# Performance work log

Measured on AMD Instinct MI355X. Metric: run time of the kernel, lower is better.

The kernel has to match this reference:

```python
import jax, jax.numpy as jnp
import numpy as np

B, S, D, H = 8, 1024, 512, 8
HD = D // H
EPS = 1e-5


def layer_norm(x, g, b):
    m = jnp.mean(x, axis=-1, keepdims=True)
    v = jnp.mean(jnp.square(x - m), axis=-1, keepdims=True)
    return (x - m) * jax.lax.rsqrt(v + EPS) * g + b


def mha(x, w_in, b_in, w_out, b_out):
    # x: [B,S,D]; w_in: [3D,D]; PyTorch MultiheadAttention math (no dropout, eval)
    b, s, d = x.shape
    qkv = x @ w_in.T + b_in                      # [B,S,3D]
    q, k, v = jnp.split(qkv, 3, axis=-1)
    q = q.reshape(b, s, H, HD)
    k = k.reshape(b, s, H, HD)
    v = v.reshape(b, s, H, HD)
    scores = jnp.einsum('bqhd,bkhd->bhqk', q, k) / np.sqrt(HD)
    a = jax.nn.softmax(scores, axis=-1)
    o = jnp.einsum('bhqk,bkhd->bqhd', a, v).reshape(b, s, d)
    return o @ w_out.T + b_out


def interp_linear(y, out_size):
    # y: [B,S_in,D]; torch F.interpolate(mode='linear', align_corners=False)
    s_in = y.shape[1]
    scale = s_in / out_size
    src = (jnp.arange(out_size, dtype=jnp.float32) + 0.5) * scale - 0.5
    src = jnp.clip(src, 0.0, s_in - 1.0)
    i0 = jnp.floor(src).astype(jnp.int32)
    i1 = jnp.minimum(i0 + 1, s_in - 1)
    w = (src - i0.astype(jnp.float32))[None, :, None]
    return y[:, i0, :] * (1.0 - w) + y[:, i1, :] * w


def setup_inputs() -> dict:
    key = jax.random.key(0)
    ks = jax.random.split(key, 16)
    sd = 0.02
    return {
        'x': jax.random.normal(ks[0], (B, S, D), jnp.float32),
        'w_in1': jax.random.normal(ks[1], (3 * D, D), jnp.float32) * sd,
        'b_in1': jnp.zeros((3 * D,), jnp.float32),
        'w_out1': jax.random.normal(ks[2], (D, D), jnp.float32) * sd,
        'b_out1': jnp.zeros((D,), jnp.float32),
        'w_in2': jax.random.normal(ks[3], (3 * D, D), jnp.float32) * sd,
        'b_in2': jnp.zeros((3 * D,), jnp.float32),
        'w_out2': jax.random.normal(ks[4], (D, D), jnp.float32) * sd,
        'b_out2': jnp.zeros((D,), jnp.float32),
        'g1': jnp.ones((D,), jnp.float32), 'beta1': jnp.zeros((D,), jnp.float32),
        'g2': jnp.ones((D,), jnp.float32), 'beta2': jnp.zeros((D,), jnp.float32),
        'g3': jnp.ones((D,), jnp.float32), 'beta3': jnp.zeros((D,), jnp.float32),
        'w_ff1': jax.random.normal(ks[5], (4 * D, D), jnp.float32) * sd,
        'b_ff1': jnp.zeros((4 * D,), jnp.float32),
        'w_ff2': jax.random.normal(ks[6], (D, 4 * D), jnp.float32) * sd,
        'b_ff2': jnp.zeros((D,), jnp.float32),
    }


def reference(x, w_in1, b_in1, w_out1, b_out1, w_in2, b_in2, w_out2, b_out2,
              g1, beta1, g2, beta2, g3, beta3, w_ff1, b_ff1, w_ff2, b_ff2):
    a1 = mha(x, w_in1, b_in1, w_out1, b_out1)
    x = layer_norm(x + a1, g1, beta1)
    # avg_pool1d kernel=2 stride=2 ceil_mode (S even -> exact halving)
    pooled = x.reshape(B, S // 2, 2, D).mean(axis=2)
    a2 = mha(pooled, w_in2, b_in2, w_out2, b_out2)
    up = interp_linear(a2, S)
    x = layer_norm(x + up, g2, beta2)
    h = jax.nn.gelu(x @ w_ff1.T + b_ff1, approximate=False)
    ff = h @ w_ff2.T + b_ff2
    return layer_norm(x + ff, g3, beta3)
```

## Files before the change

### kernel.cpp

```cpp
#include <hip/hip_runtime.h>
#include <hip/hip_bf16.h>
#include <math.h>

typedef __hip_bfloat16 bf16;
typedef __attribute__((ext_vector_type(8))) short short8;
typedef __attribute__((ext_vector_type(4))) float f32x4;
typedef __attribute__((ext_vector_type(16))) float f32x16;

__device__ __forceinline__ float ldf(const float* p, size_t i) { return p[i]; }
__device__ __forceinline__ float ldf(const bf16*  p, size_t i) { return __bfloat162float(p[i]); }
__device__ __forceinline__ void  stf(float* p, size_t i, float v) { p[i] = v; }
__device__ __forceinline__ void  stf(bf16*  p, size_t i, float v) { p[i] = __float2bfloat16(v); }

__device__ __forceinline__ float ex2(float x) { return __builtin_amdgcn_exp2f(x); }

__device__ __forceinline__ void gl16(const void* gp, void* lp) {
    __builtin_amdgcn_global_load_lds(
        (const __attribute__((address_space(1))) void*)gp,
        (__attribute__((address_space(3))) void*)lp, 16, 0, 0);
}

__device__ __forceinline__ void pl32swap(unsigned &a, unsigned &b) {
    asm volatile("v_permlane32_swap_b32 %0, %1" : "+v"(a), "+v"(b));
}

__global__ __launch_bounds__(256) void cvt_all(
    const float* __restrict__ x,
    const float* __restrict__ s0, const float* __restrict__ s1,
    const float* __restrict__ s2, const float* __restrict__ s3,
    const float* __restrict__ s4, const float* __restrict__ s5,
    bf16* __restrict__ dst)
{
    int i = blockIdx.x * 256 + threadIdx.x;
    if (i < 4194304) {
        dst[i] = __float2bfloat16(x[i]);
        return;
    }
    int j = i - 4194304;
    const float* s; int off;
    if      (j <  786432) { s = s0; off = 0; }
    else if (j < 1048576) { s = s1; off =  786432; }
    else if (j < 1835008) { s = s2; off = 1048576; }
    else if (j < 2097152) { s = s3; off = 1835008; }
    else if (j < 3145728) { s = s4; off = 2097152; }
    else                  { s = s5; off = 3145728; }
    dst[i] = __float2bfloat16(s[j - off]);
}

template <int EPI, int BN, int VS>
__global__ __launch_bounds__(256) void gemm_rs(
    const bf16* __restrict__ A, const bf16* __restrict__ W,
    const float* __restrict__ bias, bf16* __restrict__ C,
    bf16* __restrict__ vt, int M, int N, int K)
{
    constexpr int WNC = BN / 2;
    constexpr int NT  = BN / 32;
    constexpr int RB  = BN / 32;

    __shared__ __align__(16) bf16 Asl[2][128 * 64];
    __shared__ __align__(16) bf16 Bsl[2][BN * 64];

    const int tid  = threadIdx.x;
    const int lane = tid & 63;
    const int wave = tid >> 6;
    const int wm   = wave >> 1, wn = wave & 1;
    const int l15  = lane & 15, quad = lane >> 4;

    const int nwg = gridDim.x * gridDim.y;
    const int bid = blockIdx.y * gridDim.x + blockIdx.x;
    const int wid = (bid & 7) * (nwg >> 3) + (bid >> 3);
    const int bx  = wid % gridDim.x, by = wid / gridDim.x;
    const int row0 = by * 128, col0 = bx * BN;

    const int sr = tid >> 3;
    const int gg = tid & 7;

    const bf16* As[4]; const bf16* Ws[RB]; int loA[4], loB[RB];
    #pragma unroll
    for (int j = 0; j < 4; j++) {
        int row = j * 32 + sr;
        int gs  = (gg ^ (row & 7)) * 8;
        As[j]  = &A[(size_t)(row0 + row) * K + gs];
        loA[j] = row * 64 + gg * 8;
    }
    #pragma unroll
    for (int j = 0; j < RB; j++) {
        int row = j * 32 + sr;
        int gs  = (gg ^ (row & 7)) * 8;
        Ws[j]  = &W[(size_t)(col0 + row) * K + gs];
        loB[j] = row * 64 + gg * 8;
    }

    short8 ga[4], gb[RB];
    auto LOADG = [&](int k0) {
        #pragma unroll
        for (int j = 0; j < 4; j++) ga[j] = *(const short8*)(As[j] + k0);
        #pragma unroll
        for (int j = 0; j < RB; j++) gb[j] = *(const short8*)(Ws[j] + k0);
    };
    auto WRITEL = [&](int buf) {
        #pragma unroll
        for (int j = 0; j < 4; j++) *(short8*)&Asl[buf][loA[j]] = ga[j];
        #pragma unroll
        for (int j = 0; j < RB; j++) *(short8*)&Bsl[buf][loB[j]] = gb[j];
    };

    f32x4 acc[4][NT] = {};
    const int nk = K >> 6;

    LOADG(0);
    WRITEL(0);
    __syncthreads();

    int cur = 0;
    for (int i = 0; i < nk; i++) {
        if (i + 1 < nk) LOADG((i + 1) << 6);

        #pragma unroll
        for (int ks = 0; ks < 64; ks += 32) {
            short8 af[4], bfr[NT];
            const int g0 = (ks >> 3) + quad;
            const int col = (g0 ^ (l15 & 7)) * 8;
            #pragma unroll
            for (int mt = 0; mt < 4; mt++)
                af[mt] = *(const short8*)&Asl[cur][(wm * 64 + mt * 16 + l15) * 64 + col];
            #pragma unroll
            for (int nt = 0; nt < NT; nt++)
                bfr[nt] = *(const short8*)&Bsl[cur][(wn * WNC + nt * 16 + l15) * 64 + col];
            #pragma unroll
            for (int mt = 0; mt < 4; mt++)
                #pragma unroll
                for (int nt = 0; nt < NT; nt++)
                    acc[mt][nt] = __builtin_amdgcn_mfma_f32_16x16x32_bf16(
                        af[mt], bfr[nt], acc[mt][nt], 0, 0, 0);
        }

        if (i + 1 < nk) WRITEL(cur ^ 1);
        __syncthreads();
        cur ^= 1;
    }

    if constexpr (VS > 0) {
        if (col0 >= 1024) {
            constexpr int LS = (VS == 1024) ? 10 : 9;
            #pragma unroll
            for (int mt = 0; mt < 4; mt++) {
                int rowm = row0 + wm * 64 + mt * 16 + quad * 4;
                int b8 = rowm >> LS;
                int s4 = rowm & (VS - 1);
                #pragma unroll
                for (int nt = 0; nt < NT; nt++) {
                    int col = col0 + wn * WNC + nt * 16 + l15;
                    float bv = bias[col];
                    int hd = col - 1024;
                    union { bf16 b4[4]; unsigned long long u; } pk;
                    #pragma unroll
                    for (int r = 0; r < 4; r++)
                        pk.b4[r] = __float2bfloat16(acc[mt][nt][r] + bv);
                    *(unsigned long long*)&vt[
                        ((size_t)(b8 * 8 + (hd >> 6)) * 64 + (hd & 63)) * VS + s4] = pk.u;
                }
            }
            return;
        }
    }

    #pragma unroll
    for (int mt = 0; mt < 4; mt++) {
        int row = row0 + wm * 64 + mt * 16 + quad * 4;
        #pragma unroll
        for (int nt = 0; nt < NT; nt++) {
            int col = col0 + wn * WNC + nt * 16 + l15;
            float bv = bias[col];
            #pragma unroll
            for (int r = 0; r < 4; r++) {
                float v = acc[mt][nt][r] + bv;
                if (EPI == 1) v = 0.5f * v * (1.0f + erff(v * 0.70710678118654752f));
                C[(size_t)(row + r) * N + col] = __float2bfloat16(v);
            }
        }
    }
}

template <int LQB>
__global__ __launch_bounds__(128) void flash_attn_mfma(
    const bf16* __restrict__ qkv, const bf16* __restrict__ vt,
    bf16* __restrict__ o)
{
    constexpr int S   = 64 << LQB;
    constexpr int nt2 = 1 << (LQB - 1);

    __shared__ __align__(16) bf16 Kl[2][128 * 64];

    const int tid  = threadIdx.x;
    const int wave = tid >> 6, lane = tid & 63;
    const int l31  = lane & 31, hi = lane >> 5;

    const int r    = blockIdx.x;
    const int w    = (r & 7) * ((1 << LQB) * 8) + (r >> 3);
    const int qblk = w & ((1 << LQB) - 1);
    const int bh   = w >> LQB;
    const int h    = bh & 7, bb = bh >> 3;
    const int q0   = qblk * 64 + wave * 32;

    const bf16* base  = qkv + (size_t)bb * S * 1536 + h * 64;
    const bf16* vbase = vt + (size_t)bh * 64 * S;

    short8 qf[4];
    #pragma unroll
    for (int c = 0; c < 4; c++)
        qf[c] = *(const short8*)&base[(size_t)(q0 + l31) * 1536 + c * 16 + hi * 8];

    const int sr = lane >> 3;
    const int sc = ((lane & 7) ^ sr) * 8;

    auto STGK = [&](int buf, int j) {
        #pragma unroll
        for (int t = 0; t < 8; t++) {
            int r0 = wave * 64 + t * 8;
            gl16(&base[(size_t)((j << 7) + r0 + sr) * 1536 + 512 + sc],
                 &Kl[buf][r0 * 64]);
        }
    };

    f32x16 oacc[2] = {};
    float lrow = 0.f;
    const float CE = 0.18033688f;

    STGK(0, 0);

    for (int j = 0; j < nt2; j++) {
        const int cur = j & 1;
        __syncthreads();
        if (j + 1 < nt2) STGK(cur ^ 1, j + 1);

        short8 vf[2][2][2][2];
        {
            const bf16* vb = vbase + (j << 7) + hi * 8;
            #pragma unroll
            for (int dt = 0; dt < 2; dt++) {
                const bf16* vd = &vb[(size_t)(dt * 32 + l31) * S];
                #pragma unroll
                for (int t64 = 0; t64 < 2; t64++)
                    #pragma unroll
                    for (int sub = 0; sub < 2; sub++)
                        #pragma unroll
                        for (int kk = 0; kk < 2; kk++)
                            vf[t64][sub][kk][dt] =
                                *(const short8*)&vd[t64 * 64 + sub * 32 + kk * 16];
            }
        }

        #pragma unroll
        for (int t64 = 0; t64 < 2; t64++) {
            const bf16* Kc = &Kl[cur][t64 * 64 * 64];
            #pragma unroll
            for (int sub = 0; sub < 2; sub++) {
                f32x16 st = {};
                __builtin_amdgcn_s_setprio(1);
                #pragma unroll
                for (int c = 0; c < 4; c++) {
                    const int row  = sub * 32 + l31;
                    const int slot = (c * 2 + hi) ^ (row & 7);
                    short8 af = *(const short8*)&Kc[row * 64 + slot * 8];
                    st = __builtin_amdgcn_mfma_f32_32x32x16_bf16(af, qf[c], st, 0, 0, 0);
                }
                __builtin_amdgcn_s_setprio(0);

                float p[16]; float ps = 0.f;
                #pragma unroll
                for (int r2 = 0; r2 < 16; r2++) {
                    p[r2] = ex2(st[r2] * CE - 2.0f);
                    ps += p[r2];
                }
                lrow += ps;

                unsigned wk[8];
                #pragma unroll
                for (int jj = 0; jj < 8; jj++)
                    asm("v_cvt_pk_bf16_f32 %0, %1, %2"
                        : "=v"(wk[jj]) : "v"(p[2*jj]), "v"(p[2*jj+1]));

                __builtin_amdgcn_s_setprio(1);
                #pragma unroll
                for (int kk = 0; kk < 2; kk++) {
                    pl32swap(wk[kk*4+0], wk[kk*4+2]);
                    pl32swap(wk[kk*4+1], wk[kk*4+3]);
                    union { unsigned u[4]; short8 s; } pa;
                    pa.u[0] = wk[kk*4+0]; pa.u[1] = wk[kk*4+1];
                    pa.u[2] = wk[kk*4+2]; pa.u[3] = wk[kk*4+3];
                    #pragma unroll
                    for (int dt = 0; dt < 2; dt++)
                        oacc[dt] = __builtin_amdgcn_mfma_f32_32x32x16_bf16(
                            pa.s, vf[t64][sub][kk][dt], oacc[dt], 0, 0, 0);
                }
                __builtin_amdgcn_s_setprio(0);
            }
        }
    }

    lrow += __shfl_xor(lrow, 32);
    float inv = 1.0f / lrow;
    #pragma unroll
    for (int r2 = 0; r2 < 16; r2++) {
        int qr = (r2 & 3) + 8 * (r2 >> 2) + 4 * hi;
        float iv = __shfl(inv, qr);
        size_t rb = ((size_t)bb * S + q0 + qr) * 512 + h * 64;
        o[rb + l31]      = __float2bfloat16(oacc[0][r2] * iv);
        o[rb + 32 + l31] = __float2bfloat16(oacc[1][r2] * iv);
    }
}

template <typename AT, typename OT, bool INTERP>
__global__ __launch_bounds__(256) void ln_kernel(
    const AT* __restrict__ a, const bf16* __restrict__ bsrc,
    const float* __restrict__ g, const float* __restrict__ beta,
    OT* __restrict__ out)
{
    const int row = blockIdx.x;
    const int t = threadIdx.x;
    const size_t base = (size_t)row * 512;

    float a0 = ldf(a, base + t), a1 = ldf(a, base + t + 256);
    float b0, b1;
    if (INTERP) {
        int s = row & 1023, bb = row >> 10;
        float src = fminf(fmaxf((s + 0.5f) * 0.5f - 0.5f, 0.f), 511.f);
        int i0 = (int)src;
        int i1 = min(i0 + 1, 511);
        float w = src - (float)i0;
        size_t r0 = ((size_t)bb * 512 + i0) * 512;
        size_t r1 = ((size_t)bb * 512 + i1) * 512;
        b0 = __bfloat162float(bsrc[r0 + t]) * (1.f - w) + __bfloat162float(bsrc[r1 + t]) * w;
        b1 = __bfloat162float(bsrc[r0 + t + 256]) * (1.f - w) + __bfloat162float(bsrc[r1 + t + 256]) * w;
    } else {
        b0 = __bfloat162float(bsrc[base + t]);
        b1 = __bfloat162float(bsrc[base + t + 256]);
    }
    float v0 = a0 + b0, v1 = a1 + b1;

    __shared__ float red[4];
    const int lane = t & 63, wid = t >> 6;

    float sm = v0 + v1;
    #pragma unroll
    for (int off = 32; off > 0; off >>= 1) sm += __shfl_xor(sm, off);
    if (lane == 0) red[wid] = sm;
    __syncthreads();
    sm = red[0] + red[1] + red[2] + red[3];
    const float mean = sm * (1.0f / 512.0f);

    float d0 = v0 - mean, d1 = v1 - mean;
    float vv = d0 * d0 + d1 * d1;
    __syncthreads();
    #pragma unroll
    for (int off = 32; off > 0; off >>= 1) vv += __shfl_xor(vv, off);
    if (lane == 0) red[wid] = vv;
    __syncthreads();
    vv = red[0] + red[1] + red[2] + red[3];
    const float rstd = rsqrtf(vv * (1.0f / 512.0f) + 1e-5f);

    stf(out, base + t,       d0 * rstd * g[t]       + beta[t]);
    stf(out, base + t + 256, d1 * rstd * g[t + 256] + beta[t + 256]);
}

__global__ __launch_bounds__(256) void ln_pool_kernel(
    const float* __restrict__ a, const bf16* __restrict__ bsrc,
    const float* __restrict__ g, const float* __restrict__ beta,
    bf16* __restrict__ x1, bf16* __restrict__ pooled)
{
    const int pr = blockIdx.x;
    const int t = threadIdx.x;
    const size_t base0 = (size_t)(2 * pr) * 512;
    const size_t base1 = base0 + 512;

    float u0 = a[base0 + t]       + __bfloat162float(bsrc[base0 + t]);
    float u1 = a[base0 + t + 256] + __bfloat162float(bsrc[base0 + t + 256]);
    float w0 = a[base1 + t]       + __bfloat162float(bsrc[base1 + t]);
    float w1 = a[base1 + t + 256] + __bfloat162float(bsrc[base1 + t + 256]);

    __shared__ float red[2][4];
    const int lane = t & 63, wid = t >> 6;

    float s0 = u0 + u1, s1 = w0 + w1;
    #pragma unroll
    for (int off = 32; off > 0; off >>= 1) {
        s0 += __shfl_xor(s0, off);
        s1 += __shfl_xor(s1, off);
    }
    if (lane == 0) { red[0][wid] = s0; red[1][wid] = s1; }
    __syncthreads();
    const float m0 = (red[0][0] + red[0][1] + red[0][2] + red[0][3]) * (1.0f / 512.0f);
    const float m1 = (red[1][0] + red[1][1] + red[1][2] + red[1][3]) * (1.0f / 512.0f);

    float du0 = u0 - m0, du1 = u1 - m0, dw0 = w0 - m1, dw1 = w1 - m1;
    float v0 = du0 * du0 + du1 * du1, v1 = dw0 * dw0 + dw1 * dw1;
    __syncthreads();
    #pragma unroll
    for (int off = 32; off > 0; off >>= 1) {
        v0 += __shfl_xor(v0, off);
        v1 += __shfl_xor(v1, off);
    }
    if (lane == 0) { red[0][wid] = v0; red[1][wid] = v1; }
    __syncthreads();
    const float r0 = rsqrtf((red[0][0] + red[0][1] + red[0][2] + red[0][3]) * (1.0f / 512.0f) + 1e-5f);
    const float r1 = rsqrtf((red[1][0] + red[1][1] + red[1][2] + red[1][3]) * (1.0f / 512.0f) + 1e-5f);

    float g0 = g[t], g1v = g[t + 256], be0 = beta[t], be1 = beta[t + 256];
    float y00 = du0 * r0 * g0  + be0;
    float y01 = du1 * r0 * g1v + be1;
    float y10 = dw0 * r1 * g0  + be0;
    float y11 = dw1 * r1 * g1v + be1;

    x1[base0 + t]       = __float2bfloat16(y00);
    x1[base0 + t + 256] = __float2bfloat16(y01);
    x1[base1 + t]       = __float2bfloat16(y10);
    x1[base1 + t + 256] = __float2bfloat16(y11);

    const size_t pb = (size_t)pr * 512;
    pooled[pb + t]       = __float2bfloat16(0.5f * (y00 + y10));
    pooled[pb + t + 256] = __float2bfloat16(0.5f * (y01 + y11));
}

extern "C" void kernel_launch(void* const* d_in, const int* in_sizes, int n_in,
                              void* d_out, int out_size, void* d_ws, size_t ws_size,
                              hipStream_t stream)
{
    const float* x      = (const float*)d_in[0];
    const float* w_in1  = (const float*)d_in[1];
    const float* b_in1  = (const float*)d_in[2];
    const float* w_out1 = (const float*)d_in[3];
    const float* b_out1 = (const float*)d_in[4];
    const float* w_in2  = (const float*)d_in[5];
    const float* b_in2  = (const float*)d_in[6];
    const float* w_out2 = (const float*)d_in[7];
    const float* b_out2 = (const float*)d_in[8];
    const float* g1     = (const float*)d_in[9];
    const float* be1    = (const float*)d_in[10];
    const float* g2     = (const float*)d_in[11];
    const float* be2    = (const float*)d_in[12];
    const float* g3     = (const float*)d_in[13];
    const float* be3    = (const float*)d_in[14];
    const float* w_ff1  = (const float*)d_in[15];
    const float* b_ff1  = (const float*)d_in[16];
    const float* w_ff2  = (const float*)d_in[17];
    const float* b_ff2  = (const float*)d_in[18];

    bf16* ws     = (bf16*)d_ws;
    bf16* xb     = ws + 0;
    bf16* wq1    = ws + 4194304;
    bf16* wo1    = ws + 4980736;
    bf16* wq2    = ws + 5242880;
    bf16* wo2    = ws + 6029312;
    bf16* wf1    = ws + 6291456;
    bf16* wf2    = ws + 7340032;
    bf16* qkv1   = ws + 8388608;
    bf16* o1     = ws + 20971520;
    bf16* a1     = ws + 25165824;
    bf16* x1     = ws + 29360128;
    bf16* pooled = ws + 33554432;
    bf16* qkv2   = ws + 35651584;
    bf16* o2     = ws + 41943040;
    bf16* a2     = ws + 44040192;
    bf16* x2     = ws + 46137344;
    bf16* h      = ws + 8388608;
    bf16* ff     = ws + 25165824;
    bf16* vt     = ws + 46137344;

    dim3 blk(256);
    dim3 fblk(128);

    cvt_all<<<32768, blk, 0, stream>>>(x, w_in1, w_out1, w_in2, w_out2, w_ff1, w_ff2, xb);

    gemm_rs<0,128,1024><<<dim3(12, 64), blk, 0, stream>>>(xb, wq1, b_in1, qkv1, vt, 8192, 1536, 512);
    flash_attn_mfma<4><<<dim3(1024), fblk, 0, stream>>>(qkv1, vt, o1);
    gemm_rs<0,64,0><<<dim3(8, 64), blk, 0, stream>>>(o1, wo1, b_out1, a1, nullptr, 8192, 512, 512);
    ln_pool_kernel<<<4096, blk, 0, stream>>>(x, a1, g1, be1, x1, pooled);
    gemm_rs<0,64,512><<<dim3(24, 32), blk, 0, stream>>>(pooled, wq2, b_in2, qkv2, vt, 4096, 1536, 512);
    flash_attn_mfma<3><<<dim3(512), fblk, 0, stream>>>(qkv2, vt, o2);
    gemm_rs<0,64,0><<<dim3(8, 32), blk, 0, stream>>>(o2, wo2, b_out2, a2, nullptr, 4096, 512, 512);
    ln_kernel<bf16, bf16, true><<<8192, blk, 0, stream>>>(x1, a2, g2, be2, x2);
    gemm_rs<1,128,0><<<dim3(16, 64), blk, 0, stream>>>(x2, wf1, b_ff1, h, nullptr, 8192, 2048, 512);
    gemm_rs<0,64,0><<<dim3(8, 64), blk, 0, stream>>>(h, wf2, b_ff2, ff, nullptr, 8192, 512, 2048);
    ln_kernel<bf16, float, false><<<8192, blk, 0, stream>>>(x2, ff, g3, be3, (float*)d_out);
}
```

Before: 316.0 us.

## Stage V tiles through LDS alongside K with 64-key double-buffered iterations

The attention kernel now loads V^T tiles asynchronously into swizzled shared memory together with K, using 64-key tiles and double buffering. Previously each wave read V fragments straight from global memory into registers over 128-key iterations. This cuts register pressure and global-load latency on the PV matmul. The trade-off is more LDS traffic, twice as many iterations and barriers, and removal of the s_setprio hints.

```diff
diff --git a/kernel.cpp b/kernel.cpp
--- a/kernel.cpp
+++ b/kernel.cpp
@@ -187,10 +187,11 @@
     const bf16* __restrict__ qkv, const bf16* __restrict__ vt,
     bf16* __restrict__ o)
 {
-    constexpr int S   = 64 << LQB;
-    constexpr int nt2 = 1 << (LQB - 1);
-
-    __shared__ __align__(16) bf16 Kl[2][128 * 64];
+    constexpr int S  = 64 << LQB;
+    constexpr int nt = 1 << LQB;
+
+    __shared__ __align__(16) bf16 Kl[2][64 * 64];
+    __shared__ __align__(16) bf16 Vl[2][64 * 64];
 
     const int tid  = threadIdx.x;
     const int wave = tid >> 6, lane = tid & 63;
@@ -214,12 +215,16 @@
     const int sr = lane >> 3;
     const int sc = ((lane & 7) ^ sr) * 8;
 
-    auto STGK = [&](int buf, int j) {
-        #pragma unroll
-        for (int t = 0; t < 8; t++) {
-            int r0 = wave * 64 + t * 8;
-            gl16(&base[(size_t)((j << 7) + r0 + sr) * 1536 + 512 + sc],
-                 &Kl[buf][r0 * 64]);
+    auto STGKV = [&](int buf, int k0) {
+        #pragma unroll
+        for (int t = 0; t < 4; t++) {
+            int r0 = wave * 32 + t * 8;
+            gl16(&base[(size_t)(k0 + r0 + sr) * 1536 + 512 + sc], &Kl[buf][r0 * 64]);
+        }
+        #pragma unroll
+        for (int t = 0; t < 4; t++) {
+            int r0 = wave * 32 + t * 8;
+            gl16(&vbase[(size_t)(r0 + sr) * S + k0 + sc], &Vl[buf][r0 * 64]);
         }
     };
 
@@ -227,74 +232,55 @@
     float lrow = 0.f;
     const float CE = 0.18033688f;
 
-    STGK(0, 0);
-
-    for (int j = 0; j < nt2; j++) {
-        const int cur = j & 1;
+    STGKV(0, 0);
+
+    for (int it = 0; it < nt; it++) {
+        const int cur = it & 1;
         __syncthreads();
-        if (j + 1 < nt2) STGK(cur ^ 1, j + 1);
-
-        short8 vf[2][2][2][2];
-        {
-            const bf16* vb = vbase + (j << 7) + hi * 8;
-            #pragma unroll
-            for (int dt = 0; dt < 2; dt++) {
-                const bf16* vd = &vb[(size_t)(dt * 32 + l31) * S];
+        if (it + 1 < nt) STGKV(cur ^ 1, (it + 1) << 6);
+
+        const bf16* Kc = &Kl[cur][0];
+        const bf16* Vc = &Vl[cur][0];
+        #pragma unroll
+        for (int sub = 0; sub < 2; sub++) {
+            f32x16 st = {};
+            #pragma unroll
+            for (int c = 0; c < 4; c++) {
+                const int row  = sub * 32 + l31;
+                const int slot = (c * 2 + hi) ^ (row & 7);
+                short8 af = *(const short8*)&Kc[row * 64 + slot * 8];
+                st = __builtin_amdgcn_mfma_f32_32x32x16_bf16(af, qf[c], st, 0, 0, 0);
+            }
+
+            float p[16]; float ps = 0.f;
+            #pragma unroll
+            for (int r2 = 0; r2 < 16; r2++) {
+                p[r2] = ex2(st[r2] * CE - 2.0f);
+                ps += p[r2];
+            }
+            lrow += ps;
+
+            unsigned wk[8];
+            #pragma unroll
+            for (int jj = 0; jj < 8; jj++)
+                asm("v_cvt_pk_bf16_f32 %0, %1, %2"
+                    : "=v"(wk[jj]) : "v"(p[2*jj]), "v"(p[2*jj+1]));
+
+            #pragma unroll
+            for (int kk = 0; kk < 2; kk++) {
+                pl32swap(wk[kk*4+0], wk[kk*4+2]);
+                pl32swap(wk[kk*4+1], wk[kk*4+3]);
+                union { unsigned u[4]; short8 s; } pa;
+                pa.u[0] = wk[kk*4+0]; pa.u[1] = wk[kk*4+1];
+                pa.u[2] = wk[kk*4+2]; pa.u[3] = wk[kk*4+3];
                 #pragma unroll
-                for (int t64 = 0; t64 < 2; t64++)
-                    #pragma unroll
-                    for (int sub = 0; sub < 2; sub++)
-                        #pragma unroll
-                        for (int kk = 0; kk < 2; kk++)
-                            vf[t64][sub][kk][dt] =
-                                *(const short8*)&vd[t64 * 64 + sub * 32 + kk * 16];
-            }
-        }
-
-        #pragma unroll
-        for (int t64 = 0; t64 < 2; t64++) {
-            const bf16* Kc = &Kl[cur][t64 * 64 * 64];
-            #pragma unroll
-            for (int sub = 0; sub < 2; sub++) {
-                f32x16 st = {};
-                __builtin_amdgcn_s_setprio(1);
-                #pragma unroll
-                for (int c = 0; c < 4; c++) {
-                    const int row  = sub * 32 + l31;
-                    const int slot = (c * 2 + hi) ^ (row & 7);
-                    short8 af = *(const short8*)&Kc[row * 64 + slot * 8];
-                    st = __builtin_amdgcn_mfma_f32_32x32x16_bf16(af, qf[c], st, 0, 0, 0);
+                for (int dt = 0; dt < 2; dt++) {
+                    const int row  = dt * 32 + l31;
+                    const int slot = (sub * 4 + kk * 2 + hi) ^ (row & 7);
+                    short8 vf = *(const short8*)&Vc[row * 64 + slot * 8];
+                    oacc[dt] = __builtin_amdgcn_mfma_f32_32x32x16_bf16(
+                        pa.s, vf, oacc[dt], 0, 0, 0);
                 }
-                __builtin_amdgcn_s_setprio(0);
-
-                float p[16]; float ps = 0.f;
-                #pragma unroll
-                for (int r2 = 0; r2 < 16; r2++) {
-                    p[r2] = ex2(st[r2] * CE - 2.0f);
-                    ps += p[r2];
-                }
-                lrow += ps;
-
-                unsigned wk[8];
-                #pragma unroll
-                for (int jj = 0; jj < 8; jj++)
-                    asm("v_cvt_pk_bf16_f32 %0, %1, %2"
-                        : "=v"(wk[jj]) : "v"(p[2*jj]), "v"(p[2*jj+1]));
-
-                __builtin_amdgcn_s_setprio(1);
-                #pragma unroll
-                for (int kk = 0; kk < 2; kk++) {
-                    pl32swap(wk[kk*4+0], wk[kk*4+2]);
-                    pl32swap(wk[kk*4+1], wk[kk*4+3]);
-                    union { unsigned u[4]; short8 s; } pa;
-                    pa.u[0] = wk[kk*4+0]; pa.u[1] = wk[kk*4+1];
-                    pa.u[2] = wk[kk*4+2]; pa.u[3] = wk[kk*4+3];
-                    #pragma unroll
-                    for (int dt = 0; dt < 2; dt++)
-                        oacc[dt] = __builtin_amdgcn_mfma_f32_32x32x16_bf16(
-                            pa.s, vf[t64][sub][kk][dt], oacc[dt], 0, 0, 0);
-                }
-                __builtin_amdgcn_s_setprio(0);
             }
         }
     }
```

New measurement: 302.9 us. -4.1%, faster.
